# Optimization experiments

Hardware: AMD Instinct MI355X
Metric: run time of the kernel (lower is better)

## Reference

```python
import jax, jax.numpy as jnp
import numpy as np

B = 262144
Z_DIM = 128
H = 100


def setup_inputs() -> dict:
    key = jax.random.key(0)
    ks = jax.random.split(key, 7)
    x = jax.random.normal(ks[0], (B, Z_DIM), dtype=jnp.float32)
    # torch.nn.Linear default init ~ U(-1/sqrt(fan_in), 1/sqrt(fan_in)); use scaled normals
    w1 = jax.random.normal(ks[1], (H, Z_DIM), dtype=jnp.float32) / np.sqrt(Z_DIM)
    b1 = jax.random.normal(ks[2], (H,), dtype=jnp.float32) * 0.01
    w2 = jax.random.normal(ks[3], (H, H), dtype=jnp.float32) / np.sqrt(H)
    b2 = jax.random.normal(ks[4], (H,), dtype=jnp.float32) * 0.01
    w3 = jax.random.normal(ks[5], (9, H), dtype=jnp.float32) / np.sqrt(H)
    b3 = jax.random.normal(ks[6], (9,), dtype=jnp.float32) * 0.01
    return {"x": x, "w1": w1, "b1": b1, "w2": w2, "b2": b2, "w3": w3, "b3": b3}


def reference(x, w1, b1, w2, b2, w3, b3):
    h = jax.nn.relu(x @ w1.T + b1)            # [B, 100]
    h = jnp.tanh(h @ w2.T + b2)               # [B, 100]
    m = h @ w3.T + b3                         # [B, 9]
    M = m.reshape(-1, 3, 3)                   # [B, 3, 3]
    # torch.svd: M = U diag(S) V^T ; R_hat = U @ V^T == u @ vh (jax convention)
    u, s, vh = jnp.linalg.svd(M, full_matrices=False)
    R_hat = u @ vh                            # [B, 3, 3] nearest orthogonal (Procrustes)
    return R_hat.reshape(-1, 9)
```

## Files before the change

### kernel.cpp

```cpp
#include <hip/hip_runtime.h>
#include <math.h>

#define ZDIM 128
#define HDIM 100
#define JB   50

__global__ void prep_transpose(const float* __restrict__ w1,
                               const float* __restrict__ w3,
                               float* __restrict__ w1t,
                               float* __restrict__ w3t) {
    int idx = blockIdx.x * blockDim.x + threadIdx.x;
    if (idx < HDIM * ZDIM) {
        int j = idx / ZDIM;
        int k = idx - j * ZDIM;
        w1t[k * HDIM + j] = w1[idx];
    }
    if (idx < 9 * HDIM) {
        int r = idx / HDIM;
        int i = idx - r * HDIM;
        w3t[i * 9 + r] = w3[idx];
    }
}

__device__ __forceinline__ float fast_tanh(float v) {
    float e = __expf(2.0f * v);
#if __has_builtin(__builtin_amdgcn_rcpf)
    float r = __builtin_amdgcn_rcpf(e + 1.0f);
    return (e - 1.0f) * r;
#else
    return (e - 1.0f) / (e + 1.0f);
#endif
}

template<bool TR>
__global__ __launch_bounds__(256, 4) void pose_main(
    const float* __restrict__ x,
    const float* __restrict__ w1,
    const float* __restrict__ b1,
    const float* __restrict__ w2,
    const float* __restrict__ b2,
    const float* __restrict__ w3,
    const float* __restrict__ b3,
    const float* __restrict__ w1t,
    const float* __restrict__ w3t,
    float* __restrict__ out,
    int nB)
{
    int tid = blockIdx.x * blockDim.x + threadIdx.x;
    if (tid >= nB) return;

    const float4* xrow4 = reinterpret_cast<const float4*>(x + (size_t)tid * ZDIM);

    float h1[HDIM];

    #pragma unroll
    for (int jb = 0; jb < HDIM / JB; ++jb) {
        float acc[JB];
        #pragma unroll
        for (int j = 0; j < JB; ++j) acc[j] = b1[jb * JB + j];

        #pragma unroll 1
        for (int k8 = 0; k8 < ZDIM / 8; ++k8) {
            const float4 xa = xrow4[2 * k8 + 0];
            const float4 xb = xrow4[2 * k8 + 1];
            const float xs[8] = { xa.x, xa.y, xa.z, xa.w,
                                  xb.x, xb.y, xb.z, xb.w };
            #pragma unroll
            for (int kk = 0; kk < 8; ++kk) {
                const int k = k8 * 8 + kk;
                const float xv = xs[kk];
                if (TR) {
                    const float* wrow = w1t + (size_t)k * HDIM + jb * JB;
                    #pragma unroll
                    for (int j = 0; j < JB; ++j)
                        acc[j] = fmaf(xv, wrow[j], acc[j]);
                } else {
                    #pragma unroll
                    for (int j = 0; j < JB; ++j)
                        acc[j] = fmaf(xv, w1[(size_t)(jb * JB + j) * ZDIM + k], acc[j]);
                }
            }
        }
        #pragma unroll
        for (int j = 0; j < JB; ++j) h1[jb * JB + j] = fmaxf(acc[j], 0.0f);
    }

    float mr[9];
    #pragma unroll
    for (int r = 0; r < 9; ++r) mr[r] = b3[r];

    #pragma unroll 1
    for (int i = 0; i < HDIM; ++i) {
        const float* w2row = w2 + (size_t)i * HDIM;
        float a0 = 0.f, a1 = 0.f, a2 = 0.f, a3 = 0.f;
        #pragma unroll
        for (int j = 0; j < HDIM; j += 4) {
            a0 = fmaf(w2row[j + 0], h1[j + 0], a0);
            a1 = fmaf(w2row[j + 1], h1[j + 1], a1);
            a2 = fmaf(w2row[j + 2], h1[j + 2], a2);
            a3 = fmaf(w2row[j + 3], h1[j + 3], a3);
        }
        float t = fast_tanh((a0 + a1) + (a2 + a3) + b2[i]);
        #pragma unroll
        for (int r = 0; r < 9; ++r) {
            float wv = TR ? w3t[i * 9 + r] : w3[r * HDIM + i];
            mr[r] = fmaf(wv, t, mr[r]);
        }
    }

    double X00 = mr[0], X01 = mr[1], X02 = mr[2];
    double X10 = mr[3], X11 = mr[4], X12 = mr[5];
    double X20 = mr[6], X21 = mr[7], X22 = mr[8];

    #pragma unroll 1
    for (int it = 0; it < 10; ++it) {
        double C00 = X11 * X22 - X12 * X21;
        double C01 = X12 * X20 - X10 * X22;
        double C02 = X10 * X21 - X11 * X20;
        double C10 = X02 * X21 - X01 * X22;
        double C11 = X00 * X22 - X02 * X20;
        double C12 = X01 * X20 - X00 * X21;
        double C20 = X01 * X12 - X02 * X11;
        double C21 = X02 * X10 - X00 * X12;
        double C22 = X00 * X11 - X01 * X10;
        double det = X00 * C00 + X01 * C01 + X02 * C02;
        double adet = fabs(det);
        adet = adet < 1e-300 ? 1e-300 : adet;
        double sdet = (det < 0.0) ? -adet : adet;
        double nf2 = X00*X00 + X01*X01 + X02*X02
                   + X10*X10 + X11*X11 + X12*X12
                   + X20*X20 + X21*X21 + X22*X22;
        double nc2 = C00*C00 + C01*C01 + C02*C02
                   + C10*C10 + C11*C11 + C12*C12
                   + C20*C20 + C21*C21 + C22*C22;
        double g = sqrt(sqrt(nc2 / nf2) / adet);
        double a = 0.5 * g;
        double b = 0.5 / (g * sdet);
        X00 = a * X00 + b * C00;  X01 = a * X01 + b * C01;  X02 = a * X02 + b * C02;
        X10 = a * X10 + b * C10;  X11 = a * X11 + b * C11;  X12 = a * X12 + b * C12;
        X20 = a * X20 + b * C20;  X21 = a * X21 + b * C21;  X22 = a * X22 + b * C22;
    }

    float* o = out + (size_t)tid * 9;
    o[0] = (float)X00; o[1] = (float)X01; o[2] = (float)X02;
    o[3] = (float)X10; o[4] = (float)X11; o[5] = (float)X12;
    o[6] = (float)X20; o[7] = (float)X21; o[8] = (float)X22;
}

extern "C" void kernel_launch(void* const* d_in, const int* in_sizes, int n_in,
                              void* d_out, int out_size, void* d_ws, size_t ws_size,
                              hipStream_t stream) {
    const float* x  = (const float*)d_in[0];
    const float* w1 = (const float*)d_in[1];
    const float* b1 = (const float*)d_in[2];
    const float* w2 = (const float*)d_in[3];
    const float* b2 = (const float*)d_in[4];
    const float* w3 = (const float*)d_in[5];
    const float* b3 = (const float*)d_in[6];
    float* out = (float*)d_out;

    int nB = in_sizes[0] / ZDIM;

    const size_t need = (size_t)(HDIM * ZDIM + HDIM * 9) * sizeof(float);
    float* w1t = (float*)d_ws;
    float* w3t = w1t + HDIM * ZDIM;

    dim3 block(256);
    dim3 grid((nB + 255) / 256);

    if (ws_size >= need) {
        dim3 pgrid((HDIM * ZDIM + 255) / 256);
        prep_transpose<<<pgrid, block, 0, stream>>>(w1, w3, w1t, w3t);
        pose_main<true><<<grid, block, 0, stream>>>(x, w1, b1, w2, b2, w3, b3,
                                                    w1t, w3t, out, nB);
    } else {
        pose_main<false><<<grid, block, 0, stream>>>(x, w1, b1, w2, b2, w3, b3,
                                                     nullptr, nullptr, out, nB);
    }
}
```

Before: 213.1 us.

## Accumulate all 100 hidden units in one pass over x with prefetch

Layer 1 now keeps all 100 accumulators in registers and reads the x row once, instead of making two 50-wide passes that each re-read x. The next float4 of x is loaded one step ahead to hide its latency. The layer-2 loop is unrolled by 2, and fast_tanh returns to a true division instead of the hardware reciprocal. The 100 live accumulators plus h1 raise register pressure under launch_bounds(256,4), which risks spills or lower occupancy.

```diff
diff --git a/kernel.cpp b/kernel.cpp
--- a/kernel.cpp
+++ b/kernel.cpp
@@ -3,7 +3,6 @@
 
 #define ZDIM 128
 #define HDIM 100
-#define JB   50
 
 __global__ void prep_transpose(const float* __restrict__ w1,
                                const float* __restrict__ w3,
@@ -24,12 +23,7 @@
 
 __device__ __forceinline__ float fast_tanh(float v) {
     float e = __expf(2.0f * v);
-#if __has_builtin(__builtin_amdgcn_rcpf)
-    float r = __builtin_amdgcn_rcpf(e + 1.0f);
-    return (e - 1.0f) * r;
-#else
     return (e - 1.0f) / (e + 1.0f);
-#endif
 }
 
 template<bool TR>
@@ -52,44 +46,40 @@
     const float4* xrow4 = reinterpret_cast<const float4*>(x + (size_t)tid * ZDIM);
 
     float h1[HDIM];
+    #pragma unroll
+    for (int j = 0; j < HDIM; ++j) h1[j] = b1[j];
+
+    float4 cur = xrow4[0];
+    #pragma unroll 1
+    for (int k4 = 0; k4 < ZDIM / 4; ++k4) {
+        float4 nxt = xrow4[(k4 + 1) & (ZDIM / 4 - 1)];
+        const float xs[4] = { cur.x, cur.y, cur.z, cur.w };
+        #pragma unroll
+        for (int kk = 0; kk < 4; ++kk) {
+            const int k = k4 * 4 + kk;
+            const float xv = xs[kk];
+            if (TR) {
+                const float* wrow = w1t + (size_t)k * HDIM;
+                #pragma unroll
+                for (int j = 0; j < HDIM; ++j)
+                    h1[j] = fmaf(xv, wrow[j], h1[j]);
+            } else {
+                #pragma unroll
+                for (int j = 0; j < HDIM; ++j)
+                    h1[j] = fmaf(xv, w1[(size_t)j * ZDIM + k], h1[j]);
+            }
+        }
+        cur = nxt;
+    }
 
     #pragma unroll
-    for (int jb = 0; jb < HDIM / JB; ++jb) {
-        float acc[JB];
-        #pragma unroll
-        for (int j = 0; j < JB; ++j) acc[j] = b1[jb * JB + j];
-
-        #pragma unroll 1
-        for (int k8 = 0; k8 < ZDIM / 8; ++k8) {
-            const float4 xa = xrow4[2 * k8 + 0];
-            const float4 xb = xrow4[2 * k8 + 1];
-            const float xs[8] = { xa.x, xa.y, xa.z, xa.w,
-                                  xb.x, xb.y, xb.z, xb.w };
-            #pragma unroll
-            for (int kk = 0; kk < 8; ++kk) {
-                const int k = k8 * 8 + kk;
-                const float xv = xs[kk];
-                if (TR) {
-                    const float* wrow = w1t + (size_t)k * HDIM + jb * JB;
-                    #pragma unroll
-                    for (int j = 0; j < JB; ++j)
-                        acc[j] = fmaf(xv, wrow[j], acc[j]);
-                } else {
-                    #pragma unroll
-                    for (int j = 0; j < JB; ++j)
-                        acc[j] = fmaf(xv, w1[(size_t)(jb * JB + j) * ZDIM + k], acc[j]);
-                }
-            }
-        }
-        #pragma unroll
-        for (int j = 0; j < JB; ++j) h1[jb * JB + j] = fmaxf(acc[j], 0.0f);
-    }
+    for (int j = 0; j < HDIM; ++j) h1[j] = fmaxf(h1[j], 0.0f);
 
     float mr[9];
     #pragma unroll
     for (int r = 0; r < 9; ++r) mr[r] = b3[r];
 
-    #pragma unroll 1
+    #pragma unroll 2
     for (int i = 0; i < HDIM; ++i) {
         const float* w2row = w2 + (size_t)i * HDIM;
         float a0 = 0.f, a1 = 0.f, a2 = 0.f, a3 = 0.f;
```

Result: faster. 208.1 us (-2.3%).
